# Kernel optimization log

Measured on AMD Instinct MI355X. Metric: run time of the kernel, lower is better.

The kernel has to match this reference:

```python
import jax, jax.numpy as jnp
import numpy as np
import math

HIDDEN = 2048
N_HEADS = 16
N_KV = 8
HEAD_DIM = 128
EPS = 1e-6
THETA = 1000000.0
B, S = 1, 2048


def rotate_half(x):
    x1, x2 = jnp.split(x, 2, axis=-1)
    return jnp.concatenate((-x2, x1), axis=-1)


def rms_norm(x, w, eps=EPS):
    xf = x.astype(jnp.float32)
    var = jnp.mean(xf * xf, axis=-1, keepdims=True)
    return (w * (xf * jax.lax.rsqrt(var + eps)).astype(x.dtype))


def setup_inputs() -> dict:
    key = jax.random.key(0)
    ks = jax.random.split(key, 8)
    hidden_states = jax.random.normal(ks[0], (B, S, HIDDEN), dtype=jnp.float32)
    # additive causal mask: 0 on/below diagonal, -1e9 above
    causal = jnp.triu(jnp.full((S, S), -1e9, dtype=jnp.float32), k=1)
    attention_mask = causal[None, None, :, :]
    position_ids = jnp.arange(S, dtype=jnp.int64 if jax.config.jax_enable_x64 else jnp.int32)[None, :]
    sc = 0.02
    wq = jax.random.normal(ks[1], (N_HEADS * HEAD_DIM, HIDDEN), dtype=jnp.float32) * sc
    wk = jax.random.normal(ks[2], (N_KV * HEAD_DIM, HIDDEN), dtype=jnp.float32) * sc
    wv = jax.random.normal(ks[3], (N_KV * HEAD_DIM, HIDDEN), dtype=jnp.float32) * sc
    wo = jax.random.normal(ks[4], (HIDDEN, N_HEADS * HEAD_DIM), dtype=jnp.float32) * sc
    q_norm_w = jnp.ones((HEAD_DIM,), dtype=jnp.float32)
    k_norm_w = jnp.ones((HEAD_DIM,), dtype=jnp.float32)
    return {"hidden_states": hidden_states, "attention_mask": attention_mask,
            "position_ids": position_ids, "wq": wq, "wk": wk, "wv": wv,
            "wo": wo, "q_norm_w": q_norm_w, "k_norm_w": k_norm_w}


def reference(hidden_states, attention_mask, position_ids, wq, wk, wv, wo, q_norm_w, k_norm_w):
    b, s, _ = hidden_states.shape
    # projections (nn.Linear: x @ W^T)
    q = (hidden_states @ wq.T).reshape(b, s, N_HEADS, HEAD_DIM).transpose(0, 2, 1, 3)   # [b,h,s,d]
    k = (hidden_states @ wk.T).reshape(b, s, N_KV, HEAD_DIM).transpose(0, 2, 1, 3)      # [b,kv,s,d]
    v = (hidden_states @ wv.T).reshape(b, s, N_KV, HEAD_DIM).transpose(0, 2, 1, 3)
    # rotary embedding
    inv_freq = 1.0 / (THETA ** (jnp.arange(0, HEAD_DIM, 2, dtype=jnp.float32) / HEAD_DIM))  # [d/2]
    freqs = position_ids.astype(jnp.float32)[:, :, None] * inv_freq[None, None, :]          # [b,s,d/2]
    emb = jnp.concatenate((freqs, freqs), axis=-1)                                          # [b,s,d]
    cos = jnp.cos(emb)[:, None, :, :].astype(hidden_states.dtype)                           # [b,1,s,d]
    sin = jnp.sin(emb)[:, None, :, :].astype(hidden_states.dtype)
    q = q * cos + rotate_half(q) * sin
    k = k * cos + rotate_half(k) * sin
    # per-head QK RMSNorm (applied AFTER RoPE, matching source)
    q = rms_norm(q, q_norm_w)
    k = rms_norm(k, k_norm_w)
    # GQA repeat kv heads
    n_rep = N_HEADS // N_KV
    k = jnp.repeat(k, n_rep, axis=1)  # [b,h,s,d]
    v = jnp.repeat(v, n_rep, axis=1)
    # attention
    scores = jnp.einsum('bhqd,bhkd->bhqk', q, k) / math.sqrt(HEAD_DIM)
    scores = scores + attention_mask
    probs = jax.nn.softmax(scores.astype(jnp.float32), axis=-1).astype(q.dtype)
    ctx = jnp.einsum('bhqk,bhkd->bhqd', probs, v)
    ctx = ctx.transpose(0, 2, 1, 3).reshape(b, s, N_HEADS * HEAD_DIM)
    return ctx @ wo.T
```

## Files before the change

### kernel.cpp

```cpp
#include <hip/hip_runtime.h>
#include <hip/hip_bf16.h>

#define HIDDEN   2048
#define N_HEADS  16
#define N_KV     8
#define HEAD_DIM 128
#define SEQ      2048
#define EPS      1e-6f

#define BM 128
#define BN 128
#define BK 32

#define ATQ 64
#define ATK 64
#define QKS 136
#define VTS 72
#define CHUNK 16

typedef __hip_bfloat16 bf16;
typedef __bf16  bf16x8 __attribute__((ext_vector_type(8)));
typedef short   short8 __attribute__((ext_vector_type(8)));
typedef short   short4v __attribute__((ext_vector_type(4)));
typedef float   f32x4  __attribute__((ext_vector_type(4)));

typedef __attribute__((address_space(1))) void gvoid;
typedef __attribute__((address_space(3))) void lvoid;

#define ASYNC16(g, l) \
    __builtin_amdgcn_global_load_lds((gvoid*)(g), (lvoid*)(l), 16, 0, 0)

__device__ __forceinline__ short f2bfbits(float x) {
    union { bf16 h; short s; } u;
    u.h = __float2bfloat16(x);
    return u.s;
}

__global__ __launch_bounds__(256) void cvt_bf16(const float4* __restrict__ src,
                                                short4v* __restrict__ dst, int n4) {
    const int i = blockIdx.x * 256 + threadIdx.x;
    if (i >= n4) return;
    const float4 v = src[i];
    short4v p;
    p[0] = f2bfbits(v.x); p[1] = f2bfbits(v.y);
    p[2] = f2bfbits(v.z); p[3] = f2bfbits(v.w);
    dst[i] = p;
}

template <int MODE>
__device__ __forceinline__ void gemm_bf(const bf16* __restrict__ A,
                                        const bf16* __restrict__ B,
                                        float* __restrict__ C,
                                        bf16* __restrict__ Ct,
                                        int K, int ldc, int bm, int bn) {
    __shared__ __align__(16) short As[BM * BK];
    __shared__ __align__(16) short Bs[BN * BK];
    const int tid  = threadIdx.x;
    const int lane = tid & 63;
    const int wave = tid >> 6;
    const int wy   = wave & 1;
    const int wx   = wave >> 1;
    const int lrow = lane & 15;
    const int lk   = lane >> 4;
    const int srow = tid >> 2;
    const int scol = (tid & 3) * 8;

    f32x4 acc[4][4] = {};

    for (int k0 = 0; k0 < K; k0 += BK) {
        #pragma unroll
        for (int r = 0; r < 2; r++) {
            const int row = r * 64 + srow;
            ASYNC16(&A[(size_t)(bm + row) * K + k0 + scol],
                    &As[(r * 64 + wave * 16) * BK]);
            ASYNC16(&B[(size_t)(bn + row) * K + k0 + scol],
                    &Bs[(r * 64 + wave * 16) * BK]);
        }
        __syncthreads();

        short8 af[4], bfr[4];
        #pragma unroll
        for (int i = 0; i < 4; i++) {
            af[i]  = *(const short8*)&As[(wy * 64 + i * 16 + lrow) * BK + lk * 8];
            bfr[i] = *(const short8*)&Bs[(wx * 64 + i * 16 + lrow) * BK + lk * 8];
        }
        #pragma unroll
        for (int i = 0; i < 4; i++)
            #pragma unroll
            for (int j = 0; j < 4; j++)
                acc[i][j] = __builtin_amdgcn_mfma_f32_16x16x32_bf16(
                    __builtin_bit_cast(bf16x8, af[i]),
                    __builtin_bit_cast(bf16x8, bfr[j]), acc[i][j], 0, 0, 0);
        __syncthreads();
    }

    #pragma unroll
    for (int i = 0; i < 4; i++)
        #pragma unroll
        for (int j = 0; j < 4; j++) {
            if (MODE == 0) {
                #pragma unroll
                for (int v = 0; v < 4; v++)
                    C[(size_t)(bm + wy * 64 + i * 16 + lk * 4 + v) * ldc
                      + bn + wx * 64 + j * 16 + lrow] = acc[i][j][v];
            } else {
                short4v pk;
                #pragma unroll
                for (int v = 0; v < 4; v++) pk[v] = f2bfbits(acc[i][j][v]);
                *(short4v*)&Ct[(size_t)(bn + wx * 64 + j * 16 + lrow) * ldc
                               + bm + wy * 64 + i * 16 + lk * 4] = pk;
            }
        }
}

__global__ __launch_bounds__(256) void qkv_mfma(const bf16* __restrict__ x,
                                                const bf16* __restrict__ wq,
                                                const bf16* __restrict__ wk,
                                                const bf16* __restrict__ wv,
                                                float* __restrict__ Q,
                                                float* __restrict__ Kc,
                                                bf16* __restrict__ Vt) {
    const int by = blockIdx.y;
    const int bm = blockIdx.x * 128;
    if (by < 16)
        gemm_bf<0>(x, wq, Q, nullptr, HIDDEN, 2048, bm, by * 128);
    else if (by < 24)
        gemm_bf<0>(x, wk, Kc, nullptr, HIDDEN, 1024, bm, (by - 16) * 128);
    else
        gemm_bf<1>(x, wv, nullptr, Vt, HIDDEN, SEQ, bm, (by - 24) * 128);
}

__global__ __launch_bounds__(256) void oproj_mfma(const bf16* __restrict__ ctx,
                                                  const bf16* __restrict__ wo,
                                                  float* __restrict__ out) {
    gemm_bf<0>(ctx, wo, out, nullptr, N_HEADS * HEAD_DIM, HIDDEN,
               blockIdx.x * 128, blockIdx.y * 128);
}

__global__ __launch_bounds__(256) void rope_norm_kernel(
        const float* __restrict__ Q, const float* __restrict__ K,
        bf16* __restrict__ Qbf, bf16* __restrict__ Kbf,
        const float* __restrict__ qw, const float* __restrict__ kw) {
    const int s = blockIdx.x;
    const int h = blockIdx.y * 4 + (threadIdx.x >> 6);
    const int l = threadIdx.x & 63;

    const float* src;
    const float* w;
    if (h < N_HEADS) { src = Q + (size_t)s * (N_HEADS * HEAD_DIM) + h * HEAD_DIM; w = qw; }
    else             { src = K + (size_t)s * (N_KV * HEAD_DIM) + (h - N_HEADS) * HEAD_DIM; w = kw; }

    const float x1 = src[l];
    const float x2 = src[l + 64];
    const float inv_freq = exp2f((float)l * (-19.931568569324174f / 64.0f));
    const float ang = (float)s * inv_freq;
    float sn, cs;
    __sincosf(ang, &sn, &cs);
    float r1 = x1 * cs - x2 * sn;
    float r2 = x2 * cs + x1 * sn;

    float ss = r1 * r1 + r2 * r2;
    #pragma unroll
    for (int off = 1; off < 64; off <<= 1)
        ss += __shfl_xor(ss, off, 64);
    const float rs = rsqrtf(ss / 128.0f + EPS);

    if (h < N_HEADS) {
        bf16* dst = Qbf + ((size_t)s * N_HEADS + h) * HEAD_DIM;
        dst[l]      = __float2bfloat16(w[l] * r1 * rs);
        dst[l + 64] = __float2bfloat16(w[l + 64] * r2 * rs);
    } else {
        bf16* dst = Kbf + ((size_t)s * N_KV + (h - N_HEADS)) * HEAD_DIM;
        dst[l]      = __float2bfloat16(w[l] * r1 * rs);
        dst[l + 64] = __float2bfloat16(w[l + 64] * r2 * rs);
    }
}

__global__ __launch_bounds__(256) void attn_split(const bf16* __restrict__ QC,
                                                  const bf16* __restrict__ KbfG,
                                                  const bf16* __restrict__ VtG,
                                                  float* __restrict__ Opart,
                                                  float* __restrict__ Ml) {
    const int h  = blockIdx.y;
    const int bx = blockIdx.x;
    int qtile, t0, t1;
    if (bx < 16)      { qtile = bx;                 t0 = 0;  t1 = qtile; }
    else { const int idx = bx - 16; qtile = 16 + (idx >> 1);
           if (idx & 1) { t0 = 16; t1 = qtile; } else { t0 = 0; t1 = 15; } }
    const int q0    = qtile * ATQ;
    const int kvh   = h >> 1;
    const int tid   = threadIdx.x;
    const int lane  = tid & 63;
    const int w     = tid >> 6;
    const int lrow  = lane & 15;
    const int lk    = lane >> 4;
    const float scale = 0.08838834764831845f;

    __shared__ short Ks[ATK * QKS];
    __shared__ short Vt[HEAD_DIM * VTS];
    __shared__ short Ps[ATQ * VTS];

    f32x4 O[8] = {};
    float m_run[4] = {-1e30f, -1e30f, -1e30f, -1e30f};
    float l_run[4] = {};

    short8 aq[4];
    {
        const bf16* qrow =
            &QC[(size_t)(q0 + w * 16 + lrow) * (N_HEADS * HEAD_DIM) + h * HEAD_DIM];
        #pragma unroll
        for (int kc = 0; kc < 4; kc++)
            aq[kc] = *(const short8*)&qrow[kc * 32 + lk * 8];
    }

    for (int t = t0; t <= t1; t++) {
        const int k0 = t * ATK;
        for (int idx = tid; idx < ATK * 16; idx += 256) {
            const int r = idx >> 4, c8 = idx & 15;
            *(short8*)&Ks[r * QKS + c8 * 8] = *(const short8*)
                &KbfG[((size_t)(k0 + r) * N_KV + kvh) * HEAD_DIM + c8 * 8];
        }
        for (int idx = tid; idx < HEAD_DIM * 8; idx += 256) {
            const int d = idx >> 3, ck = idx & 7;
            *(short8*)&Vt[d * VTS + ck * 8] =
                *(const short8*)&VtG[((size_t)kvh * HEAD_DIM + d) * SEQ + k0 + ck * 8];
        }
        __syncthreads();

        f32x4 s[4] = {};
        #pragma unroll
        for (int nt = 0; nt < 4; nt++)
            #pragma unroll
            for (int kc = 0; kc < 4; kc++) {
                const short8 bk = *(const short8*)
                    &Ks[(nt * 16 + lrow) * QKS + kc * 32 + lk * 8];
                s[nt] = __builtin_amdgcn_mfma_f32_16x16x32_bf16(
                    __builtin_bit_cast(bf16x8, aq[kc]),
                    __builtin_bit_cast(bf16x8, bk), s[nt], 0, 0, 0);
            }

        float p[4][4];
        float mloc[4] = {-1e30f, -1e30f, -1e30f, -1e30f};
        #pragma unroll
        for (int nt = 0; nt < 4; nt++) {
            const int kglob = k0 + nt * 16 + lrow;
            #pragma unroll
            for (int r = 0; r < 4; r++) {
                float v = s[nt][r] * scale;
                v = (kglob <= q0 + w * 16 + lk * 4 + r) ? v : -1e30f;
                p[nt][r] = v;
                mloc[r] = fmaxf(mloc[r], v);
            }
        }
        #pragma unroll
        for (int off = 1; off < 16; off <<= 1)
            #pragma unroll
            for (int r = 0; r < 4; r++)
                mloc[r] = fmaxf(mloc[r], __shfl_xor(mloc[r], off, 64));

        float alpha[4], ls[4];
        #pragma unroll
        for (int r = 0; r < 4; r++) {
            const float mnew = fmaxf(m_run[r], mloc[r]);
            alpha[r] = __expf(m_run[r] - mnew);
            m_run[r] = mnew;
            ls[r] = 0.f;
        }
        #pragma unroll
        for (int nt = 0; nt < 4; nt++)
            #pragma unroll
            for (int r = 0; r < 4; r++) {
                const float e = __expf(p[nt][r] - m_run[r]);
                Ps[(w * 16 + lk * 4 + r) * VTS + nt * 16 + lrow] = f2bfbits(e);
                ls[r] += e;
            }
        #pragma unroll
        for (int off = 1; off < 16; off <<= 1)
            #pragma unroll
            for (int r = 0; r < 4; r++)
                ls[r] += __shfl_xor(ls[r], off, 64);
        #pragma unroll
        for (int r = 0; r < 4; r++)
            l_run[r] = l_run[r] * alpha[r] + ls[r];
        #pragma unroll
        for (int dnt = 0; dnt < 8; dnt++)
            #pragma unroll
            for (int r = 0; r < 4; r++)
                O[dnt][r] *= alpha[r];

        __syncthreads();

        short8 pa[2];
        #pragma unroll
        for (int ks = 0; ks < 2; ks++)
            pa[ks] = *(const short8*)&Ps[(w * 16 + lrow) * VTS + ks * 32 + lk * 8];
        #pragma unroll
        for (int dnt = 0; dnt < 8; dnt++)
            #pragma unroll
            for (int ks = 0; ks < 2; ks++) {
                const short8 vb = *(const short8*)
                    &Vt[(dnt * 16 + lrow) * VTS + ks * 32 + lk * 8];
                O[dnt] = __builtin_amdgcn_mfma_f32_16x16x32_bf16(
                    __builtin_bit_cast(bf16x8, pa[ks]),
                    __builtin_bit_cast(bf16x8, vb), O[dnt], 0, 0, 0);
            }
        __syncthreads();
    }

    const int slot = h * 48 + bx;
    #pragma unroll
    for (int r = 0; r < 4; r++) {
        const int row = w * 16 + lk * 4 + r;
        float* orow = &Opart[(size_t)slot * (ATQ * HEAD_DIM) + row * HEAD_DIM];
        #pragma unroll
        for (int dnt = 0; dnt < 8; dnt++)
            orow[dnt * 16 + lrow] = O[dnt][r];
        if (lrow == 0) {
            Ml[slot * (ATQ * 2) + row * 2]     = m_run[r];
            Ml[slot * (ATQ * 2) + row * 2 + 1] = l_run[r];
        }
    }
}

__global__ __launch_bounds__(256) void attn_combine(const float* __restrict__ Opart,
                                                    const float* __restrict__ Ml,
                                                    bf16* __restrict__ Qbf) {
    const int h   = blockIdx.y;
    const int s   = blockIdx.x * 8 + (threadIdx.x >> 5);
    const int d   = (threadIdx.x & 31) * 4;
    const int qt  = s >> 6;
    const int row = s & 63;

    int slot0, nch;
    if (qt < 16) { slot0 = h * 48 + qt;                 nch = 1; }
    else         { slot0 = h * 48 + 16 + 2 * (qt - 16); nch = 2; }

    const float m0 = Ml[slot0 * (ATQ * 2) + row * 2];
    const float l0 = Ml[slot0 * (ATQ * 2) + row * 2 + 1];
    float4 o = *(const float4*)&Opart[(size_t)slot0 * (ATQ * HEAD_DIM)
                                      + row * HEAD_DIM + d];
    float L;
    if (nch == 2) {
        const float m1 = Ml[(slot0 + 1) * (ATQ * 2) + row * 2];
        const float l1 = Ml[(slot0 + 1) * (ATQ * 2) + row * 2 + 1];
        const float4 o1 = *(const float4*)&Opart[(size_t)(slot0 + 1) * (ATQ * HEAD_DIM)
                                                 + row * HEAD_DIM + d];
        const float M  = fmaxf(m0, m1);
        const float e0 = __expf(m0 - M);
        const float e1 = __expf(m1 - M);
        L = l0 * e0 + l1 * e1;
        o.x = o.x * e0 + o1.x * e1;
        o.y = o.y * e0 + o1.y * e1;
        o.z = o.z * e0 + o1.z * e1;
        o.w = o.w * e0 + o1.w * e1;
    } else {
        L = l0;
    }
    const float inv = 1.0f / L;
    short4v pk;
    pk[0] = f2bfbits(o.x * inv); pk[1] = f2bfbits(o.y * inv);
    pk[2] = f2bfbits(o.z * inv); pk[3] = f2bfbits(o.w * inv);
    *(short4v*)&Qbf[((size_t)s * N_HEADS + h) * HEAD_DIM + d] = pk;
}

extern "C" void kernel_launch(void* const* d_in, const int* in_sizes, int n_in,
                              void* d_out, int out_size, void* d_ws, size_t ws_size,
                              hipStream_t stream) {
    const float* x   = (const float*)d_in[0];
    const float* wq  = (const float*)d_in[3];
    const float* wk  = (const float*)d_in[4];
    const float* wv  = (const float*)d_in[5];
    const float* wo  = (const float*)d_in[6];
    const float* qnw = (const float*)d_in[7];
    const float* knw = (const float*)d_in[8];

    char*  ws    = (char*)d_ws;
    float* Qw    = (float*)ws;
    bf16*  xbf   = (bf16*)(ws + (16u << 20));
    bf16*  wqbf  = (bf16*)(ws + (24u << 20));
    bf16*  wobf  = wqbf;
    bf16*  wkbf  = (bf16*)(ws + (32u << 20));
    bf16*  wvbf  = (bf16*)(ws + (36u << 20));
    bf16*  Qbf   = (bf16*)(ws + (40u << 20));
    float* Opart = (float*)ws;
    float* Ml    = (float*)(ws + (32u << 20));
    float* Kb    = (float*)d_out;
    bf16*  VtG   = (bf16*)((char*)d_out + (8u << 20));
    bf16*  KbfG  = (bf16*)((char*)d_out + (12u << 20));

    cvt_bf16<<<4096, 256, 0, stream>>>((const float4*)x,  (short4v*)xbf,  1048576);
    cvt_bf16<<<4096, 256, 0, stream>>>((const float4*)wq, (short4v*)wqbf, 1048576);
    cvt_bf16<<<2048, 256, 0, stream>>>((const float4*)wk, (short4v*)wkbf, 524288);
    cvt_bf16<<<2048, 256, 0, stream>>>((const float4*)wv, (short4v*)wvbf, 524288);

    qkv_mfma<<<dim3(SEQ / 128, 32), 256, 0, stream>>>(xbf, wqbf, wkbf, wvbf,
                                                      Qw, Kb, VtG);

    cvt_bf16<<<4096, 256, 0, stream>>>((const float4*)wo, (short4v*)wobf, 1048576);

    rope_norm_kernel<<<dim3(SEQ, 6), 256, 0, stream>>>(Qw, Kb, Qbf, KbfG, qnw, knw);

    attn_split<<<dim3(48, N_HEADS), 256, 0, stream>>>(Qbf, KbfG, VtG, Opart, Ml);

    attn_combine<<<dim3(SEQ / 8, N_HEADS), 256, 0, stream>>>(Opart, Ml, Qbf);

    oproj_mfma<<<dim3(SEQ / 128, HIDDEN / 128), 256, 0, stream>>>(Qbf, wobf,
                                                                  (float*)d_out);
}
```

Measured before the change: 322.8 us.

## Split attention KV range into 11-tile chunks and read V directly from global

Attention split-K now uses chunks of 11 KV tiles, so long query tiles are split into up to three partial blocks (63 blocks per head instead of 48), and the combine kernel merges a variable number of partials. This is meant to even out per-block work across the causal triangle. The V tile is no longer staged in shared memory; each lane loads its MFMA B operand straight from global VtG, which removes LDS stores and traffic but adds strided global loads per iteration. Workspace buffers are rearranged so that Ml lives in the output buffer and wo's bf16 copy gets its own region.

```diff
diff --git a/kernel.cpp b/kernel.cpp
--- a/kernel.cpp
+++ b/kernel.cpp
@@ -16,7 +16,8 @@
 #define ATK 64
 #define QKS 136
 #define VTS 72
-#define CHUNK 16
+#define CHT 11
+#define NBX 63
 
 typedef __hip_bfloat16 bf16;
 typedef __bf16  bf16x8 __attribute__((ext_vector_type(8)));
@@ -183,10 +184,12 @@
                                                   float* __restrict__ Ml) {
     const int h  = blockIdx.y;
     const int bx = blockIdx.x;
-    int qtile, t0, t1;
-    if (bx < 16)      { qtile = bx;                 t0 = 0;  t1 = qtile; }
-    else { const int idx = bx - 16; qtile = 16 + (idx >> 1);
-           if (idx & 1) { t0 = 16; t1 = qtile; } else { t0 = 0; t1 = 15; } }
+    int qtile, ci;
+    if (bx < 11)      { qtile = bx;                  ci = 0; }
+    else if (bx < 33) { qtile = 11 + (bx - 11) / 2;  ci = (bx - 11) & 1; }
+    else              { qtile = 22 + (bx - 33) / 3;  ci = (bx - 33) % 3; }
+    const int t0 = ci * CHT;
+    const int t1 = min(t0 + CHT - 1, qtile);
     const int q0    = qtile * ATQ;
     const int kvh   = h >> 1;
     const int tid   = threadIdx.x;
@@ -197,7 +200,6 @@
     const float scale = 0.08838834764831845f;
 
     __shared__ short Ks[ATK * QKS];
-    __shared__ short Vt[HEAD_DIM * VTS];
     __shared__ short Ps[ATQ * VTS];
 
     f32x4 O[8] = {};
@@ -212,6 +214,8 @@
         for (int kc = 0; kc < 4; kc++)
             aq[kc] = *(const short8*)&qrow[kc * 32 + lk * 8];
     }
+
+    const bf16* vbase = &VtG[((size_t)kvh * HEAD_DIM + lrow) * SEQ + lk * 8];
 
     for (int t = t0; t <= t1; t++) {
         const int k0 = t * ATK;
@@ -219,11 +223,6 @@
             const int r = idx >> 4, c8 = idx & 15;
             *(short8*)&Ks[r * QKS + c8 * 8] = *(const short8*)
                 &KbfG[((size_t)(k0 + r) * N_KV + kvh) * HEAD_DIM + c8 * 8];
-        }
-        for (int idx = tid; idx < HEAD_DIM * 8; idx += 256) {
-            const int d = idx >> 3, ck = idx & 7;
-            *(short8*)&Vt[d * VTS + ck * 8] =
-                *(const short8*)&VtG[((size_t)kvh * HEAD_DIM + d) * SEQ + k0 + ck * 8];
         }
         __syncthreads();
 
@@ -294,12 +293,12 @@
         #pragma unroll
         for (int ks = 0; ks < 2; ks++)
             pa[ks] = *(const short8*)&Ps[(w * 16 + lrow) * VTS + ks * 32 + lk * 8];
+        const bf16* vt = vbase + k0;
         #pragma unroll
         for (int dnt = 0; dnt < 8; dnt++)
             #pragma unroll
             for (int ks = 0; ks < 2; ks++) {
-                const short8 vb = *(const short8*)
-                    &Vt[(dnt * 16 + lrow) * VTS + ks * 32 + lk * 8];
+                const short8 vb = *(const short8*)&vt[(size_t)dnt * 16 * SEQ + ks * 32];
                 O[dnt] = __builtin_amdgcn_mfma_f32_16x16x32_bf16(
                     __builtin_bit_cast(bf16x8, pa[ks]),
                     __builtin_bit_cast(bf16x8, vb), O[dnt], 0, 0, 0);
@@ -307,7 +306,7 @@
         __syncthreads();
     }
 
-    const int slot = h * 48 + bx;
+    const int slot = h * NBX + bx;
     #pragma unroll
     for (int r = 0; r < 4; r++) {
         const int row = w * 16 + lk * 4 + r;
@@ -332,29 +331,29 @@
     const int row = s & 63;
 
     int slot0, nch;
-    if (qt < 16) { slot0 = h * 48 + qt;                 nch = 1; }
-    else         { slot0 = h * 48 + 16 + 2 * (qt - 16); nch = 2; }
-
-    const float m0 = Ml[slot0 * (ATQ * 2) + row * 2];
-    const float l0 = Ml[slot0 * (ATQ * 2) + row * 2 + 1];
+    if (qt < 11)      { slot0 = qt;               nch = 1; }
+    else if (qt < 22) { slot0 = 11 + 2 * (qt - 11); nch = 2; }
+    else              { slot0 = 33 + 3 * (qt - 22); nch = 3; }
+    slot0 += h * NBX;
+
+    float M = Ml[slot0 * (ATQ * 2) + row * 2];
+    float L = Ml[slot0 * (ATQ * 2) + row * 2 + 1];
     float4 o = *(const float4*)&Opart[(size_t)slot0 * (ATQ * HEAD_DIM)
                                       + row * HEAD_DIM + d];
-    float L;
-    if (nch == 2) {
-        const float m1 = Ml[(slot0 + 1) * (ATQ * 2) + row * 2];
-        const float l1 = Ml[(slot0 + 1) * (ATQ * 2) + row * 2 + 1];
-        const float4 o1 = *(const float4*)&Opart[(size_t)(slot0 + 1) * (ATQ * HEAD_DIM)
+    for (int c = 1; c < nch; c++) {
+        const float mc = Ml[(slot0 + c) * (ATQ * 2) + row * 2];
+        const float lc = Ml[(slot0 + c) * (ATQ * 2) + row * 2 + 1];
+        const float4 oc = *(const float4*)&Opart[(size_t)(slot0 + c) * (ATQ * HEAD_DIM)
                                                  + row * HEAD_DIM + d];
-        const float M  = fmaxf(m0, m1);
-        const float e0 = __expf(m0 - M);
-        const float e1 = __expf(m1 - M);
-        L = l0 * e0 + l1 * e1;
-        o.x = o.x * e0 + o1.x * e1;
-        o.y = o.y * e0 + o1.y * e1;
-        o.z = o.z * e0 + o1.z * e1;
-        o.w = o.w * e0 + o1.w * e1;
-    } else {
-        L = l0;
+        const float Mn = fmaxf(M, mc);
+        const float e0 = __expf(M - Mn);
+        const float e1 = __expf(mc - Mn);
+        L = L * e0 + lc * e1;
+        o.x = o.x * e0 + oc.x * e1;
+        o.y = o.y * e0 + oc.y * e1;
+        o.z = o.z * e0 + oc.z * e1;
+        o.w = o.w * e0 + oc.w * e1;
+        M = Mn;
     }
     const float inv = 1.0f / L;
     short4v pk;
@@ -377,14 +376,14 @@
     char*  ws    = (char*)d_ws;
     float* Qw    = (float*)ws;
     bf16*  xbf   = (bf16*)(ws + (16u << 20));
-    bf16*  wqbf  = (bf16*)(ws + (24u << 20));
-    bf16*  wobf  = wqbf;
-    bf16*  wkbf  = (bf16*)(ws + (32u << 20));
-    bf16*  wvbf  = (bf16*)(ws + (36u << 20));
-    bf16*  Qbf   = (bf16*)(ws + (40u << 20));
+    bf16*  wkbf  = (bf16*)(ws + (24u << 20));
+    bf16*  wvbf  = (bf16*)(ws + (28u << 20));
+    bf16*  wqbf  = (bf16*)(ws + (32u << 20));
+    bf16*  Qbf   = (bf16*)(ws + (32u << 20));
+    bf16*  wobf  = (bf16*)(ws + (40u << 20));
     float* Opart = (float*)ws;
-    float* Ml    = (float*)(ws + (32u << 20));
     float* Kb    = (float*)d_out;
+    float* Ml    = (float*)d_out;
     bf16*  VtG   = (bf16*)((char*)d_out + (8u << 20));
     bf16*  KbfG  = (bf16*)((char*)d_out + (12u << 20));
 
@@ -400,7 +399,7 @@
 
     rope_norm_kernel<<<dim3(SEQ, 6), 256, 0, stream>>>(Qw, Kb, Qbf, KbfG, qnw, knw);
 
-    attn_split<<<dim3(48, N_HEADS), 256, 0, stream>>>(Qbf, KbfG, VtG, Opart, Ml);
+    attn_split<<<dim3(NBX, N_HEADS), 256, 0, stream>>>(Qbf, KbfG, VtG, Opart, Ml);
 
     attn_combine<<<dim3(SEQ / 8, N_HEADS), 256, 0, stream>>>(Opart, Ml, Qbf);
 
```

Result: slower. 373.6 us (+15.7%).
